# Kernel tuning notes

Hardware: AMD Instinct MI355X
Metric: run time of the kernel (lower is better)

Reference implementation:

```python
import jax, jax.numpy as jnp
import numpy as np

OUT_H, OUT_W = 7, 7      # output_size
SCALE = 0.25             # spatial_scale
SR = 2                   # sampling_ratio


def setup_inputs() -> dict:
    key = jax.random.key(0)
    k1, k2, k3, k4 = jax.random.split(key, 4)
    B, C, T, H, W = 2, 256, 16, 64, 64
    x = jax.random.normal(k1, (B, C, T, H, W), dtype=jnp.float32)
    K = 128
    ids = jax.random.randint(k2, (K,), 0, B).astype(jnp.float32)
    xy = jax.random.uniform(k3, (K, 2), minval=0.0, maxval=200.0, dtype=jnp.float32)
    wh = jax.random.uniform(k4, (K, 2), minval=16.0, maxval=56.0, dtype=jnp.float32)
    # rois = [batch_id, x1, y1, x2, y2] as produced by convert_to_roi_format
    rois = jnp.concatenate([ids[:, None], xy, xy + wh], axis=1)
    return {"x": x, "rois": rois}


def _roi_align_3d(x, rois, out_h, out_w, scale, sr):
    """maskrcnn-benchmark style (aligned=False) RoIAlign applied to every
    temporal slice of a [B,C,T,H,W] feature map. Returns [K,C,T,out_h,out_w]."""
    B, C, T, H, W = x.shape
    Hf = jnp.float32(H)
    Wf = jnp.float32(W)

    def one_roi(roi):
        b = roi[0].astype(jnp.int32)
        feat = jnp.take(x, b, axis=0)  # [C,T,H,W]
        x1, y1, x2, y2 = roi[1] * scale, roi[2] * scale, roi[3] * scale, roi[4] * scale
        roi_w = jnp.maximum(x2 - x1, 1.0)
        roi_h = jnp.maximum(y2 - y1, 1.0)
        # sample point coordinates (sr samples per bin)
        xs = x1 + (jnp.arange(out_w * sr, dtype=jnp.float32) + 0.5) * (roi_w / (out_w * sr))
        ys = y1 + (jnp.arange(out_h * sr, dtype=jnp.float32) + 0.5) * (roi_h / (out_h * sr))
        # out-of-bounds samples contribute zero (CUDA kernel semantics)
        my = (ys >= -1.0) & (ys <= Hf)
        mx = (xs >= -1.0) & (xs <= Wf)
        yc = jnp.clip(ys, 0.0, Hf - 1.0)
        xc = jnp.clip(xs, 0.0, Wf - 1.0)
        y0 = jnp.clip(jnp.floor(yc).astype(jnp.int32), 0, H - 2)
        x0 = jnp.clip(jnp.floor(xc).astype(jnp.int32), 0, W - 2)
        ly = yc - y0.astype(jnp.float32)  # in [0,1]
        lx = xc - x0.astype(jnp.float32)
        hy, hx = 1.0 - ly, 1.0 - lx
        Y0 = y0[:, None]
        X0 = x0[None, :]
        # bilinear interpolation over all C,T at once -> [C,T,P,Q]
        v = (feat[:, :, Y0, X0] * (hy[:, None] * hx[None, :])
             + feat[:, :, Y0, X0 + 1] * (hy[:, None] * lx[None, :])
             + feat[:, :, Y0 + 1, X0] * (ly[:, None] * hx[None, :])
             + feat[:, :, Y0 + 1, X0 + 1] * (ly[:, None] * lx[None, :]))
        v = v * (my[:, None] & mx[None, :]).astype(feat.dtype)
        # average the sr x sr samples in each bin -> [C,T,out_h,out_w]
        return v.reshape(C, T, out_h, sr, out_w, sr).mean(axis=(3, 5))

    return jax.vmap(one_roi)(rois)


def reference(x, rois):
    return _roi_align_3d(x, rois, OUT_H, OUT_W, SCALE, SR)
```

## Files before the change

kernel.cpp:

```cpp
#include <hip/hip_runtime.h>


#define LP  68
#define LPH 34
#define PLW (65 * LP)

__global__ __launch_bounds__(128) void pooler_pre(const float* __restrict__ rois,
                                                  int* __restrict__ wi) {
    __shared__ int sb[128];
    int tid = threadIdx.x;
    sb[tid] = (int)rois[5 * tid];
    __syncthreads();
    if (tid == 0) {
        int c0 = 0, c1 = 0;
        for (int j = 0; j < 128; ++j) {
            if (sb[j] == 0) wi[2 + c0++] = j;
            else            wi[2 + 128 + c1++] = j;
        }
        wi[0] = c0; wi[1] = c1;
        for (int j = c0; j < 128; ++j) wi[2 + j] = 0;
        for (int j = c1; j < 128; ++j) wi[2 + 128 + j] = 0;
    }
}

__global__ __launch_bounds__(512) void pooler_main(const float* __restrict__ x,
                                                   const float* __restrict__ rois,
                                                   const int* __restrict__ wi,
                                                   float* __restrict__ out) {
    __shared__ float plane[2][PLW];
    __shared__ float rb[128][4];
    __shared__ int   rlist[128];
    __shared__ int   snroi;

    const int tid = threadIdx.x;
    const int bid = blockIdx.x;
    const int b   = bid >> 11;
    const int c   = (bid >> 3) & 255;
    const int tp  = bid & 7;

    const float4* src = (const float4*)(x + ((((size_t)b * 256 + c) * 16 + 2 * tp) << 12));
    #pragma unroll
    for (int j = 0; j < 4; ++j) {
        int g = tid + j * 512;
        float4 v = src[g];
        int pi = g >> 10, gg = g & 1023;
        *(float4*)&plane[pi][(gg >> 4) * LP + ((gg & 15) << 2)] = v;
    }
    if (tid < 162) {
        int pi = tid >= 81, u = pi ? tid - 81 : tid;
        float4 z = make_float4(0.f, 0.f, 0.f, 0.f);
        if (u < 65) *(float4*)&plane[pi][u * LP + 64] = z;
        else        *(float4*)&plane[pi][64 * LP + ((u - 65) << 2)] = z;
    }
    if (tid < 128) {
        int j = wi[2 + (b << 7) + tid];
        rlist[tid] = j;
        float x1 = rois[5 * j + 1] * 0.25f, y1 = rois[5 * j + 2] * 0.25f;
        float x2 = rois[5 * j + 3] * 0.25f, y2 = rois[5 * j + 4] * 0.25f;
        rb[tid][0] = x1;
        rb[tid][1] = y1;
        rb[tid][2] = fmaxf(x2 - x1, 1.0f) * (1.0f / 14.0f);
        rb[tid][3] = fmaxf(y2 - y1, 1.0f) * (1.0f / 14.0f);
        if (tid == 0) snroi = wi[b];
    }
    __syncthreads();

    const int nroi  = snroi;
    const int ntask = nroi * 14;
    const size_t obase0 = ((size_t)c * 16 + 2 * tp) * 49;

    for (int task = tid; task < ntask; task += 512) {
        int r    = task / 14;
        int rem  = task - r * 14;
        int half = rem / 7;
        int ph   = rem - half * 7;
        int k = rlist[r];
        float x1 = rb[r][0], y1 = rb[r][1], bw = rb[r][2], bh = rb[r][3];

        float ys0 = fmaf((float)(2 * ph) + 0.5f, bh, y1);
        float ys1 = ys0 + bh;
        float my0 = (ys0 >= -1.0f && ys0 <= 64.0f) ? 1.0f : 0.0f;
        float my1 = (ys1 >= -1.0f && ys1 <= 64.0f) ? 1.0f : 0.0f;
        float yc0 = fminf(fmaxf(ys0, 0.0f), 63.0f);
        float yc1 = fminf(fmaxf(ys1, 0.0f), 63.0f);
        int y00 = min((int)yc0, 62);
        int y01 = min((int)yc1, 62);
        float ly0 = yc0 - (float)y00, ly1 = yc1 - (float)y01;
        float h0 = (1.0f - ly0) * my0, l0 = ly0 * my0;
        float h1 = (1.0f - ly1) * my1, l1 = ly1 * my1;
        bool dy = (y01 != y00);
        float yw0 = h0 + (dy ? 0.0f : h1);
        float yw1 = l0 + (dy ? h1 : l1);
        float yw2 = dy ? l1 : 0.0f;
        const float2* prow = (const float2*)plane[half] + y00 * LPH;

        const size_t ob = (((size_t)k << 12) + (obase0 >> 0) / 49 * 0 + 0) * 49
                        + obase0 + (size_t)half * 49 + ph * 7;
        #pragma unroll
        for (int pw = 0; pw < 7; ++pw) {
            float xs0 = fmaf((float)(2 * pw) + 0.5f, bw, x1);
            float xs1 = xs0 + bw;
            float mx0 = (xs0 >= -1.0f && xs0 <= 64.0f) ? 0.25f : 0.0f;
            float mx1 = (xs1 >= -1.0f && xs1 <= 64.0f) ? 0.25f : 0.0f;
            float xc0 = fminf(fmaxf(xs0, 0.0f), 63.0f);
            float xc1 = fminf(fmaxf(xs1, 0.0f), 63.0f);
            int x00 = min((int)xc0, 62);
            int x01 = min((int)xc1, 62);
            float lx0 = xc0 - (float)x00, lx1 = xc1 - (float)x01;
            float a0 = (1.0f - lx0) * mx0, b0w = lx0 * mx0;
            float a1 = (1.0f - lx1) * mx1, b1w = lx1 * mx1;
            bool dx = (x01 != x00);
            float xw0 = a0  + (dx ? 0.0f : a1);
            float xw1 = b0w + (dx ? a1 : b1w);
            float xw2 = dx ? b1w : 0.0f;
            bool odd = (x00 & 1);
            float w0 = odd ? 0.0f : xw0;
            float w1 = odd ? xw0 : xw1;
            float w2 = odd ? xw1 : xw2;
            float w3 = odd ? xw2 : 0.0f;
            int xb2 = x00 >> 1;

            float2 r0a = prow[xb2],           r0b = prow[xb2 + 1];
            float2 r1a = prow[xb2 + LPH],     r1b = prow[xb2 + LPH + 1];
            float2 r2a = prow[xb2 + 2 * LPH], r2b = prow[xb2 + 2 * LPH + 1];
            float s0 = w0 * r0a.x + w1 * r0a.y + w2 * r0b.x + w3 * r0b.y;
            float s1 = w0 * r1a.x + w1 * r1a.y + w2 * r1b.x + w3 * r1b.y;
            float s2 = w0 * r2a.x + w1 * r2a.y + w2 * r2b.x + w3 * r2b.y;
            out[ob + pw] = yw0 * s0 + yw1 * s1 + yw2 * s2;
        }
    }
}

extern "C" void kernel_launch(void* const* d_in, const int* in_sizes, int n_in,
                              void* d_out, int out_size, void* d_ws, size_t ws_size,
                              hipStream_t stream) {
    const float* x    = (const float*)d_in[0];
    const float* rois = (const float*)d_in[1];
    float* out = (float*)d_out;
    int*   wi  = (int*)d_ws;
    pooler_pre<<<1, 128, 0, stream>>>(rois, wi);
    pooler_main<<<2 * 256 * 8, 512, 0, stream>>>(x, rois, wi, out);
}
```

Before: 70.21 us.

## Precompute per-ROI bilinear weight tables in pre-kernel, one plane per block

The pre-kernel now computes, once per ROI, the row and column offsets and bilinear weights for every output bin, packing the weights as fp16 pairs into a workspace table. Each main block copies that table into shared memory and does only loads and packed FMAs, so the coordinate and weight arithmetic is no longer repeated for every channel and time slice. Blocks now hold one plane instead of two, which doubles the grid and uses a smaller row pad. Storing the weights in fp16 lowers accuracy, and every block pays for a roughly 21 KB table load from global memory.

```diff
diff --git a/kernel.cpp b/kernel.cpp
--- a/kernel.cpp
+++ b/kernel.cpp
@@ -1,90 +1,36 @@
 #include <hip/hip_runtime.h>
+#include <hip/hip_fp16.h>
 
 
-#define LP  68
-#define LPH 34
-#define PLW (65 * LP)
+#define LP   66
+#define ROWB 264
+
+typedef float v2f __attribute__((ext_vector_type(2)));
+
+__device__ inline v2f h2f(unsigned u) {
+    __half2 h = __builtin_bit_cast(__half2, u);
+    float2 f = __half22float2(h);
+    return v2f{f.x, f.y};
+}
 
 __global__ __launch_bounds__(128) void pooler_pre(const float* __restrict__ rois,
-                                                  int* __restrict__ wi) {
+                                                  unsigned* __restrict__ wt) {
     __shared__ int sb[128];
-    int tid = threadIdx.x;
-    sb[tid] = (int)rois[5 * tid];
-    __syncthreads();
-    if (tid == 0) {
-        int c0 = 0, c1 = 0;
-        for (int j = 0; j < 128; ++j) {
-            if (sb[j] == 0) wi[2 + c0++] = j;
-            else            wi[2 + 128 + c1++] = j;
-        }
-        wi[0] = c0; wi[1] = c1;
-        for (int j = c0; j < 128; ++j) wi[2 + j] = 0;
-        for (int j = c1; j < 128; ++j) wi[2 + 128 + j] = 0;
-    }
-}
-
-__global__ __launch_bounds__(512) void pooler_main(const float* __restrict__ x,
-                                                   const float* __restrict__ rois,
-                                                   const int* __restrict__ wi,
-                                                   float* __restrict__ out) {
-    __shared__ float plane[2][PLW];
-    __shared__ float rb[128][4];
-    __shared__ int   rlist[128];
-    __shared__ int   snroi;
-
-    const int tid = threadIdx.x;
-    const int bid = blockIdx.x;
-    const int b   = bid >> 11;
-    const int c   = (bid >> 3) & 255;
-    const int tp  = bid & 7;
-
-    const float4* src = (const float4*)(x + ((((size_t)b * 256 + c) * 16 + 2 * tp) << 12));
-    #pragma unroll
-    for (int j = 0; j < 4; ++j) {
-        int g = tid + j * 512;
-        float4 v = src[g];
-        int pi = g >> 10, gg = g & 1023;
-        *(float4*)&plane[pi][(gg >> 4) * LP + ((gg & 15) << 2)] = v;
-    }
-    if (tid < 162) {
-        int pi = tid >= 81, u = pi ? tid - 81 : tid;
-        float4 z = make_float4(0.f, 0.f, 0.f, 0.f);
-        if (u < 65) *(float4*)&plane[pi][u * LP + 64] = z;
-        else        *(float4*)&plane[pi][64 * LP + ((u - 65) << 2)] = z;
-    }
-    if (tid < 128) {
-        int j = wi[2 + (b << 7) + tid];
-        rlist[tid] = j;
-        float x1 = rois[5 * j + 1] * 0.25f, y1 = rois[5 * j + 2] * 0.25f;
-        float x2 = rois[5 * j + 3] * 0.25f, y2 = rois[5 * j + 4] * 0.25f;
-        rb[tid][0] = x1;
-        rb[tid][1] = y1;
-        rb[tid][2] = fmaxf(x2 - x1, 1.0f) * (1.0f / 14.0f);
-        rb[tid][3] = fmaxf(y2 - y1, 1.0f) * (1.0f / 14.0f);
-        if (tid == 0) snroi = wi[b];
-    }
-    __syncthreads();
-
-    const int nroi  = snroi;
-    const int ntask = nroi * 14;
-    const size_t obase0 = ((size_t)c * 16 + 2 * tp) * 49;
-
-    for (int task = tid; task < ntask; task += 512) {
-        int r    = task / 14;
-        int rem  = task - r * 14;
-        int half = rem / 7;
-        int ph   = rem - half * 7;
-        int k = rlist[r];
-        float x1 = rb[r][0], y1 = rb[r][1], bw = rb[r][2], bh = rb[r][3];
-
-        float ys0 = fmaf((float)(2 * ph) + 0.5f, bh, y1);
+    const int k = threadIdx.x;
+    float x1 = rois[5 * k + 1] * 0.25f, y1 = rois[5 * k + 2] * 0.25f;
+    float x2 = rois[5 * k + 3] * 0.25f, y2 = rois[5 * k + 4] * 0.25f;
+    float bw = fmaxf(x2 - x1, 1.0f) * (1.0f / 14.0f);
+    float bh = fmaxf(y2 - y1, 1.0f) * (1.0f / 14.0f);
+    sb[k] = (int)rois[5 * k];
+    for (int i = 0; i < 7; ++i) {
+        int e = k * 7 + i;
+        float ys0 = fmaf((float)(2 * i) + 0.5f, bh, y1);
         float ys1 = ys0 + bh;
         float my0 = (ys0 >= -1.0f && ys0 <= 64.0f) ? 1.0f : 0.0f;
         float my1 = (ys1 >= -1.0f && ys1 <= 64.0f) ? 1.0f : 0.0f;
         float yc0 = fminf(fmaxf(ys0, 0.0f), 63.0f);
         float yc1 = fminf(fmaxf(ys1, 0.0f), 63.0f);
-        int y00 = min((int)yc0, 62);
-        int y01 = min((int)yc1, 62);
+        int y00 = min((int)yc0, 62), y01 = min((int)yc1, 62);
         float ly0 = yc0 - (float)y00, ly1 = yc1 - (float)y01;
         float h0 = (1.0f - ly0) * my0, l0 = ly0 * my0;
         float h1 = (1.0f - ly1) * my1, l1 = ly1 * my1;
@@ -92,41 +38,107 @@
         float yw0 = h0 + (dy ? 0.0f : h1);
         float yw1 = l0 + (dy ? h1 : l1);
         float yw2 = dy ? l1 : 0.0f;
-        const float2* prow = (const float2*)plane[half] + y00 * LPH;
+        wt[e]        = (unsigned)(y00 * ROWB);
+        wt[896 + e]  = __builtin_bit_cast(unsigned, __halves2half2(__float2half(yw0), __float2half(yw1)));
+        wt[1792 + e] = __builtin_bit_cast(unsigned, __halves2half2(__float2half(yw2), __float2half(0.0f)));
+        float xs0 = fmaf((float)(2 * i) + 0.5f, bw, x1);
+        float xs1 = xs0 + bw;
+        float mx0 = (xs0 >= -1.0f && xs0 <= 64.0f) ? 0.25f : 0.0f;
+        float mx1 = (xs1 >= -1.0f && xs1 <= 64.0f) ? 0.25f : 0.0f;
+        float xc0 = fminf(fmaxf(xs0, 0.0f), 63.0f);
+        float xc1 = fminf(fmaxf(xs1, 0.0f), 63.0f);
+        int x00 = min((int)xc0, 62), x01 = min((int)xc1, 62);
+        float lx0 = xc0 - (float)x00, lx1 = xc1 - (float)x01;
+        float a0 = (1.0f - lx0) * mx0, b0 = lx0 * mx0;
+        float a1 = (1.0f - lx1) * mx1, b1 = lx1 * mx1;
+        bool dx = (x01 != x00);
+        float xw0 = a0 + (dx ? 0.0f : a1);
+        float xw1 = b0 + (dx ? a1 : b1);
+        float xw2 = dx ? b1 : 0.0f;
+        bool odd = (x00 & 1);
+        float w0 = odd ? 0.0f : xw0;
+        float w1 = odd ? xw0 : xw1;
+        float w2 = odd ? xw1 : xw2;
+        float w3 = odd ? xw2 : 0.0f;
+        wt[2688 + e] = (unsigned)((x00 >> 1) * 8);
+        wt[3584 + e] = __builtin_bit_cast(unsigned, __halves2half2(__float2half(w0), __float2half(w1)));
+        wt[4480 + e] = __builtin_bit_cast(unsigned, __halves2half2(__float2half(w2), __float2half(w3)));
+    }
+    __syncthreads();
+    if (k == 0) {
+        int c0 = 0, c1 = 0;
+        for (int j = 0; j < 128; ++j) {
+            if (sb[j] == 0) wt[5378 + c0++] = j;
+            else            wt[5378 + 128 + c1++] = j;
+        }
+        wt[5376] = c0; wt[5377] = c1;
+        for (int j = c0; j < 128; ++j) wt[5378 + j] = 0;
+        for (int j = c1; j < 128; ++j) wt[5378 + 128 + j] = 0;
+    }
+}
 
-        const size_t ob = (((size_t)k << 12) + (obase0 >> 0) / 49 * 0 + 0) * 49
-                        + obase0 + (size_t)half * 49 + ph * 7;
+__global__ __launch_bounds__(512, 8) void pooler_main(const float* __restrict__ x,
+                                                      const unsigned* __restrict__ wt,
+                                                      float* __restrict__ out) {
+    __shared__ __align__(16) unsigned tab[5376];
+    __shared__ __align__(16) float plane[65 * LP];
+    __shared__ int rlist[128];
+    __shared__ int snroi;
+
+    const int tid = threadIdx.x;
+    const int bid = blockIdx.x;
+    const int b   = bid >> 12;
+
+    const float4* src = (const float4*)(x + ((size_t)bid << 12));
+    #pragma unroll
+    for (int j = 0; j < 2; ++j) {
+        int g = tid + j * 512;
+        float4 v = src[g];
+        float* d = &plane[(g >> 4) * LP + ((g & 15) << 2)];
+        ((float2*)d)[0] = make_float2(v.x, v.y);
+        ((float2*)d)[1] = make_float2(v.z, v.w);
+    }
+    if (tid < 98) {
+        if (tid < 65) { plane[tid * LP + 64] = 0.f; plane[tid * LP + 65] = 0.f; }
+        else { int c2 = (tid - 65) * 2; plane[64 * LP + c2] = 0.f; plane[64 * LP + c2 + 1] = 0.f; }
+    }
+    #pragma unroll
+    for (int j = 0; j < 3; ++j) {
+        int g = tid + j * 512;
+        if (g < 1344) ((float4*)tab)[g] = ((const float4*)wt)[g];
+    }
+    if (tid < 128) rlist[tid] = (int)wt[5378 + (b << 7) + tid];
+    if (tid == 0)  snroi = (int)wt[5376 + b];
+    __syncthreads();
+
+    const int pl = bid & 4095;
+    const int ntask = snroi * 7;
+    for (int task = tid; task < ntask; task += 512) {
+        int r  = task / 7;
+        int ph = task - r * 7;
+        int k  = rlist[r];
+        int ye = k * 7 + ph;
+        unsigned yoff = tab[ye];
+        v2f yab = h2f(tab[896 + ye]);
+        v2f ycd = h2f(tab[1792 + ye]);
+        const char* prow = (const char*)plane + yoff;
+        float* po = out + ((size_t)((k << 12) | pl)) * 49 + ph * 7;
         #pragma unroll
         for (int pw = 0; pw < 7; ++pw) {
-            float xs0 = fmaf((float)(2 * pw) + 0.5f, bw, x1);
-            float xs1 = xs0 + bw;
-            float mx0 = (xs0 >= -1.0f && xs0 <= 64.0f) ? 0.25f : 0.0f;
-            float mx1 = (xs1 >= -1.0f && xs1 <= 64.0f) ? 0.25f : 0.0f;
-            float xc0 = fminf(fmaxf(xs0, 0.0f), 63.0f);
-            float xc1 = fminf(fmaxf(xs1, 0.0f), 63.0f);
-            int x00 = min((int)xc0, 62);
-            int x01 = min((int)xc1, 62);
-            float lx0 = xc0 - (float)x00, lx1 = xc1 - (float)x01;
-            float a0 = (1.0f - lx0) * mx0, b0w = lx0 * mx0;
-            float a1 = (1.0f - lx1) * mx1, b1w = lx1 * mx1;
-            bool dx = (x01 != x00);
-            float xw0 = a0  + (dx ? 0.0f : a1);
-            float xw1 = b0w + (dx ? a1 : b1w);
-            float xw2 = dx ? b1w : 0.0f;
-            bool odd = (x00 & 1);
-            float w0 = odd ? 0.0f : xw0;
-            float w1 = odd ? xw0 : xw1;
-            float w2 = odd ? xw1 : xw2;
-            float w3 = odd ? xw2 : 0.0f;
-            int xb2 = x00 >> 1;
-
-            float2 r0a = prow[xb2],           r0b = prow[xb2 + 1];
-            float2 r1a = prow[xb2 + LPH],     r1b = prow[xb2 + LPH + 1];
-            float2 r2a = prow[xb2 + 2 * LPH], r2b = prow[xb2 + 2 * LPH + 1];
-            float s0 = w0 * r0a.x + w1 * r0a.y + w2 * r0b.x + w3 * r0b.y;
-            float s1 = w0 * r1a.x + w1 * r1a.y + w2 * r1b.x + w3 * r1b.y;
-            float s2 = w0 * r2a.x + w1 * r2a.y + w2 * r2b.x + w3 * r2b.y;
-            out[ob + pw] = yw0 * s0 + yw1 * s1 + yw2 * s2;
+            int xe = k * 7 + pw;
+            const char* p = prow + tab[2688 + xe];
+            v2f w01 = h2f(tab[3584 + xe]);
+            v2f w23 = h2f(tab[4480 + xe]);
+            v2f r0a = *(const v2f*)p,              r0b = *(const v2f*)(p + 8);
+            v2f r1a = *(const v2f*)(p + ROWB),     r1b = *(const v2f*)(p + ROWB + 8);
+            v2f r2a = *(const v2f*)(p + 2 * ROWB), r2b = *(const v2f*)(p + 2 * ROWB + 8);
+            v2f s0 = __builtin_elementwise_fma(r0b, w23, r0a * w01);
+            v2f s1 = __builtin_elementwise_fma(r1b, w23, r1a * w01);
+            v2f s2 = __builtin_elementwise_fma(r2b, w23, r2a * w01);
+            v2f acc = s0 * v2f{yab.x, yab.x};
+            acc = __builtin_elementwise_fma(s1, v2f{yab.y, yab.y}, acc);
+            acc = __builtin_elementwise_fma(s2, v2f{ycd.x, ycd.x}, acc);
+            po[pw] = acc.x + acc.y;
         }
     }
 }
@@ -137,7 +149,7 @@
     const float* x    = (const float*)d_in[0];
     const float* rois = (const float*)d_in[1];
     float* out = (float*)d_out;
-    int*   wi  = (int*)d_ws;
-    pooler_pre<<<1, 128, 0, stream>>>(rois, wi);
-    pooler_main<<<2 * 256 * 8, 512, 0, stream>>>(x, rois, wi, out);
+    unsigned* wt = (unsigned*)d_ws;
+    pooler_pre<<<1, 128, 0, stream>>>(rois, wt);
+    pooler_main<<<2 * 256 * 16, 512, 0, stream>>>(x, wt, out);
 }
```

After: 75.40 us. 7.4% more time.
